# Kernel optimization log

Measured on AMD Instinct MI355X. Metric: run time of the kernel, lower is better.

The kernel has to match this reference:

```python
import jax, jax.numpy as jnp
import numpy as np

K = 16  # neighbors, from self.k in the module


def _pconv(x, w, b):
    # 1x1 Conv1d: x (B,C,N), w (O,C), b (O,)
    return jnp.einsum('oc,bcn->bon', w, x) + b[None, :, None]


def _gather_neighbors(xn, idx):
    # xn (B,N,C), idx (B,N,K) int -> (B,N,K,C)
    return jax.vmap(lambda xb, ib: xb[ib])(xn, idx)


def _local_maxpool(x, idx):
    # x (B,C,N) -> (B,N,C): max over K gathered neighbor features
    xn = jnp.transpose(x, (0, 2, 1))
    return jnp.max(_gather_neighbors(xn, idx), axis=2)


def setup_inputs() -> dict:
    key = jax.random.key(0)
    ks = jax.random.split(key, 20)
    B, N = 8, 2048
    def w(k, shape, fan_in):
        return jax.random.normal(k, shape, dtype=jnp.float32) / np.sqrt(fan_in)
    inp = {
        'pts': jax.random.normal(ks[0], (B, N, 3), dtype=jnp.float32),
        'w1a': w(ks[1], (64, 12), 12), 'b1a': jnp.zeros((64,), jnp.float32),
        'w1b': w(ks[2], (64, 64), 64), 'b1b': jnp.zeros((64,), jnp.float32),
        'w1c': w(ks[3], (64, 64), 64), 'b1c': jnp.zeros((64,), jnp.float32),
        'lin1_w': w(ks[4], (64, 64), 64), 'lin1_b': jnp.zeros((64,), jnp.float32),
        'conv1_w': w(ks[5], (128, 64), 64), 'conv1_b': jnp.zeros((128,), jnp.float32),
        'lin2_w': w(ks[6], (128, 128), 128), 'lin2_b': jnp.zeros((128,), jnp.float32),
        'conv2_w': w(ks[7], (1024, 128), 128), 'conv2_b': jnp.zeros((1024,), jnp.float32),
        'w2a': w(ks[8], (512, 1024), 1024), 'b2a': jnp.zeros((512,), jnp.float32),
        'w2b': w(ks[9], (512, 512), 512), 'b2b': jnp.zeros((512,), jnp.float32),
    }
    return inp


def reference(pts, w1a, b1a, w1b, b1b, w1c, b1c, lin1_w, lin1_b,
              conv1_w, conv1_b, lin2_w, lin2_b, conv2_w, conv2_b,
              w2a, b2a, w2b, b2b):
    B, N, _ = pts.shape
    pts_t = jnp.transpose(pts, (0, 2, 1))  # (B,3,N)
    # kNN: topk of negative squared pairwise distance (self is first neighbor)
    sq = jnp.sum(pts_t * pts_t, axis=1)                      # (B,N)
    inner = jnp.einsum('bdn,bdm->bnm', pts_t, pts_t)         # (B,N,N)
    neg_dist = 2.0 * inner - sq[:, :, None] - sq[:, None, :]
    idx = jax.lax.top_k(neg_dist, K)[1]                      # (B,N,K) int32
    # local_cov: outer product of first two gathered neighbor coords
    neigh = _gather_neighbors(pts, idx)                      # (B,N,K,3)
    cov = jnp.einsum('bni,bnj->bnij', neigh[:, :, 0], neigh[:, :, 1])
    cov = cov.reshape(B, N, 9)
    x = jnp.concatenate([pts_t, jnp.transpose(cov, (0, 2, 1))], axis=1)  # (B,12,N)
    # mlp1
    x = jax.nn.relu(_pconv(x, w1a, b1a))
    x = jax.nn.relu(_pconv(x, w1b, b1b))
    x = jax.nn.relu(_pconv(x, w1c, b1c))
    # graph layer
    x = _local_maxpool(x, idx)                               # (B,N,64)
    x = x @ lin1_w.T + lin1_b                                # (B,N,64)
    x = jnp.transpose(x, (0, 2, 1))                          # (B,64,N)
    x = jax.nn.relu(_pconv(x, conv1_w, conv1_b))             # (B,128,N)
    x = _local_maxpool(x, idx)                               # (B,N,128)
    x = x @ lin2_w.T + lin2_b
    x = jnp.transpose(x, (0, 2, 1))                          # (B,128,N)
    x = _pconv(x, conv2_w, conv2_b)                          # (B,1024,N)
    # global max pool
    x = jnp.max(x, axis=2, keepdims=True)                    # (B,1024,1)
    # mlp2
    x = jax.nn.relu(_pconv(x, w2a, b2a))
    x = _pconv(x, w2b, b2b)                                  # (B,512,1)
    return jnp.transpose(x, (0, 2, 1))                       # (B,1,512)
```

## Files before the change

kernel.cpp:

```cpp
#include <hip/hip_runtime.h>

#define BB 8
#define NN 2048
#define KK 16
#define QT 64
#define NSLICE 8
#define SLEN 256
#define KP 18

typedef short bf16x8 __attribute__((ext_vector_type(8)));
typedef float f32x4 __attribute__((ext_vector_type(4)));
typedef unsigned short ushort8v __attribute__((ext_vector_type(8)));

__device__ __forceinline__ float4 f4max(float4 a, float4 b) {
  return make_float4(fmaxf(a.x, b.x), fmaxf(a.y, b.y), fmaxf(a.z, b.z), fmaxf(a.w, b.w));
}

__device__ __forceinline__ unsigned short f2bf(float x) {
  union { float f; unsigned u; } v; v.f = x;
  unsigned r = v.u + 0x7fffu + ((v.u >> 16) & 1u);
  return (unsigned short)(r >> 16);
}
__device__ __forceinline__ float bf2f(unsigned short h) {
  union { unsigned u; float f; } v; v.u = ((unsigned)h) << 16;
  return v.f;
}

__global__ __launch_bounds__(512) void knn_kernel(
    const float* __restrict__ pts, int* __restrict__ knn_idx,
    const float* __restrict__ lin1_w, const float* __restrict__ lin1_b,
    const float* __restrict__ conv1_w, const float* __restrict__ conv1_b,
    const float* __restrict__ lin2_w, const float* __restrict__ lin2_b,
    const float* __restrict__ conv2_w, const float* __restrict__ conv2_b,
    unsigned short* __restrict__ w1hi, unsigned short* __restrict__ w1lo,
    float* __restrict__ b1p,
    unsigned short* __restrict__ w2hi, unsigned short* __restrict__ w2lo,
    float* __restrict__ b2p) {
  __shared__ float4 sp[NN];
  __shared__ unsigned char  pk[NSLICE][QT][KP];
  __shared__ float          s1v[4][QT][17];
  __shared__ unsigned short s1i[4][QT][17];
  const int tid = threadIdx.x;

  if (blockIdx.x >= 256) {
    const int gt = (blockIdx.x - 256) * 512 + tid;
    if (gt < 8192) {
      const int o = gt >> 6, c = gt & 63;
      float acc = 0.f;
#pragma unroll 8
      for (int k = 0; k < 64; ++k) acc += conv1_w[o * 64 + k] * lin1_w[k * 64 + c];
      const unsigned short h = f2bf(acc);
      w1hi[o * 64 + c] = h;
      w1lo[o * 64 + c] = f2bf(acc - bf2f(h));
      if (c == 0) {
        float bb = conv1_b[o];
        for (int k = 0; k < 64; ++k) bb += conv1_w[o * 64 + k] * lin1_b[k];
        b1p[o] = bb;
      }
    } else if (gt < 8192 + 131072) {
      const int t2 = gt - 8192;
      const int o = t2 >> 7, c = t2 & 127;
      float acc = 0.f;
#pragma unroll 8
      for (int k = 0; k < 128; ++k) acc += conv2_w[o * 128 + k] * lin2_w[k * 128 + c];
      const unsigned short h = f2bf(acc);
      w2hi[o * 128 + c] = h;
      w2lo[o * 128 + c] = f2bf(acc - bf2f(h));
      if (c == 0) {
        float bb = conv2_b[o];
        for (int k = 0; k < 128; ++k) bb += conv2_w[o * 128 + k] * lin2_b[k];
        b2p[o] = bb;
      }
    }
    return;
  }

  const int b = blockIdx.x & 7;
  const int tile = blockIdx.x >> 3;
  const int q = tid & 63;
  const int s = tid >> 6;

  for (int i = tid; i < NN; i += 512) {
    float x = pts[(size_t)(b * NN + i) * 3 + 0];
    float y = pts[(size_t)(b * NN + i) * 3 + 1];
    float z = pts[(size_t)(b * NN + i) * 3 + 2];
    sp[i] = make_float4(x, y, z, x * x + y * y + z * z);
  }
  __syncthreads();

  {
    const float4 pq = sp[tile * QT + q];
    const float qx = 2.f * pq.x, qy = 2.f * pq.y, qz = 2.f * pq.z;
    unsigned qk[KP];
#pragma unroll
    for (int j = 0; j < KP; ++j) qk[j] = 0u;
    const int m0 = s * SLEN;
    for (int mb = 0; mb < SLEN; mb += 8) {
      float4 c[8];
#pragma unroll
      for (int u = 0; u < 8; ++u) c[u] = sp[m0 + mb + u];
#pragma unroll
      for (int u = 0; u < 8; ++u) {
        const float v = fmaf(qx, c[u].x, fmaf(qy, c[u].y, fmaf(qz, c[u].z, -c[u].w)));
        unsigned uu = __float_as_uint(v);
        unsigned key = uu ^ ((unsigned)(((int)uu) >> 31) | 0x80000000u);
        unsigned run = (key & 0xFFFFFF00u) | (unsigned)(255 - (mb + u));
#pragma unroll
        for (int j = 0; j < KP; ++j) {
          const unsigned hi = max(qk[j], run);
          const unsigned lo = min(qk[j], run);
          qk[j] = hi; run = lo;
        }
      }
    }
#pragma unroll
    for (int j = 0; j < KP; ++j) pk[s][q][j] = (unsigned char)(qk[j] & 0xFFu);
  }
  __syncthreads();

  if (tid < 256) {
    const int q2 = tid & 63, pr = tid >> 6;
    const float4 pm = sp[tile * QT + q2];
    const float qx = 2.f * pm.x, qy = 2.f * pm.y, qz = 2.f * pm.z;
    float mv[16]; int mi[16];
#pragma unroll
    for (int j = 0; j < 16; ++j) { mv[j] = -3.0e38f; mi[j] = 0; }
#pragma unroll 1
    for (int ss = 2 * pr; ss <= 2 * pr + 1; ++ss) {
      const int base = ss * SLEN;
#pragma unroll 1
      for (int j = 0; j < KP; ++j) {
        const int id = base + 255 - (int)pk[ss][q2][j];
        const float4 c = sp[id];
        const float v = fmaf(qx, c.x, fmaf(qy, c.y, fmaf(qz, c.z, -c.w)));
        if (v <= mv[15]) break;
        mv[15] = v; mi[15] = id;
#pragma unroll
        for (int t = 15; t > 0; --t) {
          if (mv[t] > mv[t - 1]) {
            float tv = mv[t]; mv[t] = mv[t - 1]; mv[t - 1] = tv;
            int ti = mi[t]; mi[t] = mi[t - 1]; mi[t - 1] = ti;
          }
        }
      }
    }
#pragma unroll
    for (int j = 0; j < 16; ++j) {
      s1v[pr][q2][j] = mv[j];
      s1i[pr][q2][j] = (unsigned short)mi[j];
    }
  }
  __syncthreads();

  if (tid < QT) {
    float mv[16]; int mi[16];
#pragma unroll
    for (int j = 0; j < 16; ++j) { mv[j] = -3.0e38f; mi[j] = 0; }
#pragma unroll 1
    for (int pr = 0; pr < 4; ++pr) {
#pragma unroll 1
      for (int j = 0; j < 16; ++j) {
        const float v = s1v[pr][tid][j];
        if (v <= mv[15]) break;
        const int id = s1i[pr][tid][j];
        mv[15] = v; mi[15] = id;
#pragma unroll
        for (int t = 15; t > 0; --t) {
          if (mv[t] > mv[t - 1]) {
            float tv = mv[t]; mv[t] = mv[t - 1]; mv[t - 1] = tv;
            int ti = mi[t]; mi[t] = mi[t - 1]; mi[t - 1] = ti;
          }
        }
      }
    }
    const int nq = tile * QT + tid;
#pragma unroll
    for (int j = 0; j < 16; ++j) knn_idx[(size_t)(b * NN + nq) * KK + j] = mi[j];
  }
}

__global__ __launch_bounds__(512, 2) void mlp1_kernel(
    const float* __restrict__ pts, const int* __restrict__ knn_idx,
    const float* __restrict__ w1a, const float* __restrict__ b1a,
    const float* __restrict__ w1b, const float* __restrict__ b1b,
    const float* __restrict__ w1c, const float* __restrict__ b1c,
    float* __restrict__ f1) {
  __shared__ float h1[64][64];
  __shared__ float h2[64][64];
  const int tid = threadIdx.x;
  const int p = tid & 63;
  const int ch = tid >> 6;
  const int b = blockIdx.x & 7;
  const int nc = blockIdx.x >> 3;
  const int bn = b * NN + nc * 64 + p;

  const int n0 = knn_idx[(size_t)bn * KK + 0];
  const int n1 = knn_idx[(size_t)bn * KK + 1];
  const float* pp = &pts[(size_t)bn * 3];
  const float* p0 = &pts[((size_t)(b << 11) + n0) * 3];
  const float* p1 = &pts[((size_t)(b << 11) + n1) * 3];
  float in[12];
  in[0] = pp[0]; in[1] = pp[1]; in[2] = pp[2];
  {
    float a0 = p0[0], a1 = p0[1], a2 = p0[2];
    float c0 = p1[0], c1 = p1[1], c2 = p1[2];
    in[3] = a0 * c0; in[4]  = a0 * c1; in[5]  = a0 * c2;
    in[6] = a1 * c0; in[7]  = a1 * c1; in[8]  = a1 * c2;
    in[9] = a2 * c0; in[10] = a2 * c1; in[11] = a2 * c2;
  }

#pragma unroll
  for (int oi = 0; oi < 8; ++oi) {
    const int o = ch * 8 + oi;
    float a = b1a[o];
#pragma unroll
    for (int c = 0; c < 12; ++c) a += w1a[o * 12 + c] * in[c];
    h1[o][p] = fmaxf(a, 0.f);
  }
  __syncthreads();

  {
    float acc[8];
#pragma unroll
    for (int oi = 0; oi < 8; ++oi) acc[oi] = b1b[ch * 8 + oi];
#pragma unroll 1
    for (int cc = 0; cc < 64; cc += 32) {
      float xr[32];
#pragma unroll
      for (int c = 0; c < 32; ++c) xr[c] = h1[cc + c][p];
#pragma unroll
      for (int oi = 0; oi < 8; ++oi) {
        const int o = ch * 8 + oi;
#pragma unroll
        for (int c = 0; c < 32; ++c) acc[oi] += w1b[o * 64 + cc + c] * xr[c];
      }
    }
    __syncthreads();
#pragma unroll
    for (int oi = 0; oi < 8; ++oi) h2[ch * 8 + oi][p] = fmaxf(acc[oi], 0.f);
  }
  __syncthreads();

  {
    float acc[8];
#pragma unroll
    for (int oi = 0; oi < 8; ++oi) acc[oi] = b1c[ch * 8 + oi];
#pragma unroll 1
    for (int cc = 0; cc < 64; cc += 32) {
      float xr[32];
#pragma unroll
      for (int c = 0; c < 32; ++c) xr[c] = h2[cc + c][p];
#pragma unroll
      for (int oi = 0; oi < 8; ++oi) {
        const int o = ch * 8 + oi;
#pragma unroll
        for (int c = 0; c < 32; ++c) acc[oi] += w1c[o * 64 + cc + c] * xr[c];
      }
    }
#pragma unroll
    for (int oi = 0; oi < 8; ++oi)
      f1[(size_t)bn * 64 + ch * 8 + oi] = fmaxf(acc[oi], 0.f);
  }
}

__global__ __launch_bounds__(256, 2) void gconv1_kernel(
    const float* __restrict__ f1, const int* __restrict__ knn_idx,
    const unsigned short* __restrict__ w1hi, const unsigned short* __restrict__ w1lo,
    const float* __restrict__ b1p, float* __restrict__ f2) {
  __shared__ __align__(16) unsigned short xls[2][64][64];
  const int b = blockIdx.x & 7, nc = blockIdx.x >> 3;
  const int tid = threadIdx.x;
  const int lane = tid & 63, wv = tid >> 6;

  {
    const int p = tid & 63, ch = tid >> 6;
    const int bn = b * NN + nc * 64 + p;
    const int4* idr = (const int4*)&knn_idx[(size_t)bn * KK];
    int4 nb4[4];
#pragma unroll
    for (int q = 0; q < 4; ++q) nb4[q] = idr[q];
    float4 mx[4];
#pragma unroll
    for (int q = 0; q < 4; ++q) mx[q] = make_float4(-3e38f, -3e38f, -3e38f, -3e38f);
#pragma unroll
    for (int j = 0; j < KK; ++j) {
      const int nb = (j & 3) == 0 ? nb4[j >> 2].x : (j & 3) == 1 ? nb4[j >> 2].y
                   : (j & 3) == 2 ? nb4[j >> 2].z : nb4[j >> 2].w;
      const float4* v = (const float4*)&f1[((size_t)(b << 11) + nb) * 64 + ch * 16];
#pragma unroll
      for (int q = 0; q < 4; ++q) mx[q] = f4max(mx[q], v[q]);
    }
    char* basep = (char*)&xls[0][0][0];
#pragma unroll
    for (int s = 0; s < 2; ++s) {
      float xv[8] = {mx[2 * s].x, mx[2 * s].y, mx[2 * s].z, mx[2 * s].w,
                     mx[2 * s + 1].x, mx[2 * s + 1].y, mx[2 * s + 1].z, mx[2 * s + 1].w};
      ushort8v hw, lw;
#pragma unroll
      for (int j = 0; j < 8; ++j) {
        unsigned short h = f2bf(xv[j]);
        hw[j] = h;
        lw[j] = f2bf(xv[j] - bf2f(h));
      }
      const int slot = ch * 2 + s;
      const int swz = slot ^ (p & 7);
      char* dst = basep + p * 128 + swz * 16;
      *(ushort8v*)dst = hw;
      *(ushort8v*)(dst + 8192) = lw;
    }
  }
  __syncthreads();

  const int g = lane >> 4, r = lane & 15;
  const char* basep = (const char*)&xls[0][0][0];
  bf16x8 ah[4][2], al[4][2];
#pragma unroll
  for (int m = 0; m < 4; ++m) {
    const int row = m * 16 + r;
#pragma unroll
    for (int kt = 0; kt < 2; ++kt) {
      const int swz = (kt * 4 + g) ^ (row & 7);
      const char* p = basep + row * 128 + swz * 16;
      ah[m][kt] = *(const bf16x8*)p;
      al[m][kt] = *(const bf16x8*)(p + 8192);
    }
  }
  f32x4 acc[4][2];
#pragma unroll
  for (int m = 0; m < 4; ++m)
#pragma unroll
    for (int nt = 0; nt < 2; ++nt) acc[m][nt] = (f32x4){0.f, 0.f, 0.f, 0.f};

#pragma unroll
  for (int nt = 0; nt < 2; ++nt) {
    const int o = (wv * 2 + nt) * 16 + r;
    const char* wb = (const char*)w1hi + (size_t)o * 128 + g * 16;
    const char* lb = (const char*)w1lo + (size_t)o * 128 + g * 16;
    bf16x8 bh[2], bl[2];
#pragma unroll
    for (int kt = 0; kt < 2; ++kt) {
      bh[kt] = *(const bf16x8*)(wb + kt * 64);
      bl[kt] = *(const bf16x8*)(lb + kt * 64);
    }
#pragma unroll
    for (int kt = 0; kt < 2; ++kt) {
#pragma unroll
      for (int m = 0; m < 4; ++m) {
        acc[m][nt] = __builtin_amdgcn_mfma_f32_16x16x32_bf16(ah[m][kt], bh[kt], acc[m][nt], 0, 0, 0);
        acc[m][nt] = __builtin_amdgcn_mfma_f32_16x16x32_bf16(ah[m][kt], bl[kt], acc[m][nt], 0, 0, 0);
        acc[m][nt] = __builtin_amdgcn_mfma_f32_16x16x32_bf16(al[m][kt], bh[kt], acc[m][nt], 0, 0, 0);
      }
    }
  }
#pragma unroll
  for (int nt = 0; nt < 2; ++nt) {
    const int o = (wv * 2 + nt) * 16 + r;
    const float bias = b1p[o];
#pragma unroll
    for (int m = 0; m < 4; ++m) {
#pragma unroll
      for (int j = 0; j < 4; ++j) {
        const int row = m * 16 + g * 4 + j;
        f2[((size_t)(b * NN + nc * 64 + row)) * 128 + o] = fmaxf(acc[m][nt][j] + bias, 0.f);
      }
    }
  }
}

__global__ __launch_bounds__(256, 2) void gconv2max_kernel(
    const float* __restrict__ f2, const int* __restrict__ knn_idx,
    const unsigned short* __restrict__ w2hi, const unsigned short* __restrict__ w2lo,
    float* __restrict__ pmax) {
  __shared__ __align__(16) unsigned short xls[2][64][128];
  const int b = blockIdx.x & 7, nc = blockIdx.x >> 3;
  const int tid = threadIdx.x;
  const int lane = tid & 63, wv = tid >> 6;

  {
    const int p = tid & 63, ch = tid >> 6;
    const int bn = b * NN + nc * 64 + p;
    const int4* idr = (const int4*)&knn_idx[(size_t)bn * KK];
    int4 nb4[4];
#pragma unroll
    for (int q = 0; q < 4; ++q) nb4[q] = idr[q];
    float4 mx[8];
#pragma unroll
    for (int q = 0; q < 8; ++q) mx[q] = make_float4(-3e38f, -3e38f, -3e38f, -3e38f);
#pragma unroll
    for (int j = 0; j < KK; ++j) {
      const int nb = (j & 3) == 0 ? nb4[j >> 2].x : (j & 3) == 1 ? nb4[j >> 2].y
                   : (j & 3) == 2 ? nb4[j >> 2].z : nb4[j >> 2].w;
      const float4* v = (const float4*)&f2[((size_t)(b << 11) + nb) * 128 + ch * 32];
#pragma unroll
      for (int q = 0; q < 8; ++q) mx[q] = f4max(mx[q], v[q]);
    }
    char* basep = (char*)&xls[0][0][0];
#pragma unroll
    for (int s = 0; s < 4; ++s) {
      float xv[8] = {mx[2 * s].x, mx[2 * s].y, mx[2 * s].z, mx[2 * s].w,
                     mx[2 * s + 1].x, mx[2 * s + 1].y, mx[2 * s + 1].z, mx[2 * s + 1].w};
      ushort8v hw, lw;
#pragma unroll
      for (int j = 0; j < 8; ++j) {
        unsigned short h = f2bf(xv[j]);
        hw[j] = h;
        lw[j] = f2bf(xv[j] - bf2f(h));
      }
      const int slot = ch * 4 + s;
      const int swz = slot ^ (p & 15);
      char* dst = basep + p * 256 + swz * 16;
      *(ushort8v*)dst = hw;
      *(ushort8v*)(dst + 16384) = lw;
    }
  }
  __syncthreads();

  const int g = lane >> 4, r = lane & 15;
  const char* basep = (const char*)&xls[0][0][0];
  float omax[16];
#pragma unroll
  for (int ot = 0; ot < 16; ++ot) omax[ot] = -3e38f;

#pragma unroll
  for (int mg = 0; mg < 2; ++mg) {
    bf16x8 ah[2][4], al[2][4];
#pragma unroll
    for (int m = 0; m < 2; ++m) {
      const int row = (mg * 2 + m) * 16 + r;
#pragma unroll
      for (int kt = 0; kt < 4; ++kt) {
        const int swz = (kt * 4 + g) ^ (row & 15);
        const char* p = basep + row * 256 + swz * 16;
        ah[m][kt] = *(const bf16x8*)p;
        al[m][kt] = *(const bf16x8*)(p + 16384);
      }
    }
#pragma unroll 1
    for (int ot = 0; ot < 16; ++ot) {
      const int o = wv * 256 + ot * 16 + r;
      const char* wb = (const char*)w2hi + (size_t)o * 256 + g * 16;
      const char* lb = (const char*)w2lo + (size_t)o * 256 + g * 16;
      bf16x8 bh[4], bl[4];
#pragma unroll
      for (int kt = 0; kt < 4; ++kt) {
        bh[kt] = *(const bf16x8*)(wb + kt * 64);
        bl[kt] = *(const bf16x8*)(lb + kt * 64);
      }
      f32x4 acc0 = {0.f, 0.f, 0.f, 0.f}, acc1 = {0.f, 0.f, 0.f, 0.f};
#pragma unroll
      for (int kt = 0; kt < 4; ++kt) {
        acc0 = __builtin_amdgcn_mfma_f32_16x16x32_bf16(ah[0][kt], bh[kt], acc0, 0, 0, 0);
        acc1 = __builtin_amdgcn_mfma_f32_16x16x32_bf16(ah[1][kt], bh[kt], acc1, 0, 0, 0);
        acc0 = __builtin_amdgcn_mfma_f32_16x16x32_bf16(ah[0][kt], bl[kt], acc0, 0, 0, 0);
        acc1 = __builtin_amdgcn_mfma_f32_16x16x32_bf16(ah[1][kt], bl[kt], acc1, 0, 0, 0);
        acc0 = __builtin_amdgcn_mfma_f32_16x16x32_bf16(al[0][kt], bh[kt], acc0, 0, 0, 0);
        acc1 = __builtin_amdgcn_mfma_f32_16x16x32_bf16(al[1][kt], bh[kt], acc1, 0, 0, 0);
      }
      float mx = fmaxf(fmaxf(fmaxf(acc0[0], acc0[1]), fmaxf(acc0[2], acc0[3])),
                       fmaxf(fmaxf(acc1[0], acc1[1]), fmaxf(acc1[2], acc1[3])));
      omax[ot] = fmaxf(omax[ot], mx);
    }
  }
#pragma unroll
  for (int ot = 0; ot < 16; ++ot) {
    float v = omax[ot];
    v = fmaxf(v, __shfl_xor(v, 16, 64));
    v = fmaxf(v, __shfl_xor(v, 32, 64));
    omax[ot] = v;
  }
  if (lane < 16) {
#pragma unroll
    for (int ot = 0; ot < 16; ++ot) {
      const int o = wv * 256 + ot * 16 + lane;
      pmax[((size_t)b * 1024 + o) * 32 + nc] = omax[ot];
    }
  }
}

__global__ __launch_bounds__(256) void head_g_kernel(
    const float* __restrict__ pmax, const float* __restrict__ b2p,
    float* __restrict__ gbuf) {
  const int b = blockIdx.x & 7;
  const int o = (blockIdx.x >> 3) * 256 + threadIdx.x;
  const float4* p = (const float4*)&pmax[((size_t)b * 1024 + o) * 32];
  float4 a4 = p[0];
#pragma unroll
  for (int gi = 1; gi < 8; ++gi) a4 = f4max(a4, p[gi]);
  gbuf[b * 1024 + o] = fmaxf(fmaxf(a4.x, a4.y), fmaxf(a4.z, a4.w)) + b2p[o];
}

__global__ __launch_bounds__(256) void head_a_kernel(
    const float* __restrict__ gbuf, const float* __restrict__ w2a,
    const float* __restrict__ b2a, float* __restrict__ hbuf) {
  const int b = blockIdx.x & 7;
  const int k = (blockIdx.x >> 3) * 4 + (threadIdx.x >> 6);
  const int lane = threadIdx.x & 63;
  const float4* wr = (const float4*)&w2a[(size_t)k * 1024];
  const float4* gv = (const float4*)&gbuf[b * 1024];
  float a = 0.f;
#pragma unroll
  for (int i = 0; i < 4; ++i) {
    float4 w = wr[lane + i * 64], xx = gv[lane + i * 64];
    a += w.x * xx.x + w.y * xx.y + w.z * xx.z + w.w * xx.w;
  }
#pragma unroll
  for (int s = 32; s >= 1; s >>= 1) a += __shfl_xor(a, s, 64);
  if (lane == 0) hbuf[b * 512 + k] = fmaxf(a + b2a[k], 0.f);
}

__global__ __launch_bounds__(256) void head_b_kernel(
    const float* __restrict__ hbuf, const float* __restrict__ w2b,
    const float* __restrict__ b2b, float* __restrict__ out) {
  const int b = blockIdx.x & 7;
  const int k = (blockIdx.x >> 3) * 4 + (threadIdx.x >> 6);
  const int lane = threadIdx.x & 63;
  const float4* wr = (const float4*)&w2b[(size_t)k * 512];
  const float4* hv = (const float4*)&hbuf[b * 512];
  float a = 0.f;
#pragma unroll
  for (int i = 0; i < 2; ++i) {
    float4 w = wr[lane + i * 64], xx = hv[lane + i * 64];
    a += w.x * xx.x + w.y * xx.y + w.z * xx.z + w.w * xx.w;
  }
#pragma unroll
  for (int s = 32; s >= 1; s >>= 1) a += __shfl_xor(a, s, 64);
  if (lane == 0) out[b * 512 + k] = a + b2b[k];
}

extern "C" void kernel_launch(void* const* d_in, const int* in_sizes, int n_in,
                              void* d_out, int out_size, void* d_ws, size_t ws_size,
                              hipStream_t stream) {
  const float* pts     = (const float*)d_in[0];
  const float* w1a     = (const float*)d_in[1];
  const float* b1a     = (const float*)d_in[2];
  const float* w1b     = (const float*)d_in[3];
  const float* b1b     = (const float*)d_in[4];
  const float* w1c     = (const float*)d_in[5];
  const float* b1c     = (const float*)d_in[6];
  const float* lin1_w  = (const float*)d_in[7];
  const float* lin1_b  = (const float*)d_in[8];
  const float* conv1_w = (const float*)d_in[9];
  const float* conv1_b = (const float*)d_in[10];
  const float* lin2_w  = (const float*)d_in[11];
  const float* lin2_b  = (const float*)d_in[12];
  const float* conv2_w = (const float*)d_in[13];
  const float* conv2_b = (const float*)d_in[14];
  const float* w2a     = (const float*)d_in[15];
  const float* b2a     = (const float*)d_in[16];
  const float* w2b     = (const float*)d_in[17];
  const float* b2b     = (const float*)d_in[18];

  char* ws = (char*)d_ws;
  int*   knn_idx = (int*)ws;
  float* f1  = (float*)(ws + (1u << 20));
  float* pm  = (float*)(ws + (5u << 20));
  unsigned short* w2hi = (unsigned short*)(ws + (6u << 20));
  unsigned short* w2lo = (unsigned short*)(ws + (6u << 20) + (1u << 18));
  unsigned short* w1hi = (unsigned short*)(ws + (6u << 20) + (2u << 18));
  unsigned short* w1lo = (unsigned short*)(ws + (6u << 20) + (2u << 18) + (1u << 14));
  float* b1p = (float*)(ws + (6u << 20) + (2u << 18) + (2u << 14));
  float* b2p = (float*)(ws + (6u << 20) + (2u << 18) + (3u << 14));
  float* gbuf = (float*)(ws + (7u << 20));
  float* hbuf = (float*)(ws + (7u << 20) + (1u << 16));
  float* f2  = (float*)(ws + (9u << 20));

  knn_kernel   <<<544, 512, 0, stream>>>(pts, knn_idx,
                                         lin1_w, lin1_b, conv1_w, conv1_b,
                                         lin2_w, lin2_b, conv2_w, conv2_b,
                                         w1hi, w1lo, b1p, w2hi, w2lo, b2p);
  mlp1_kernel  <<<256, 512, 0, stream>>>(pts, knn_idx, w1a, b1a, w1b, b1b, w1c, b1c, f1);
  gconv1_kernel<<<256, 256, 0, stream>>>(f1, knn_idx, w1hi, w1lo, b1p, f2);
  gconv2max_kernel<<<256, 256, 0, stream>>>(f2, knn_idx, w2hi, w2lo, pm);
  head_g_kernel<<<32, 256, 0, stream>>>(pm, b2p, gbuf);
  head_a_kernel<<<1024, 256, 0, stream>>>(gbuf, w2a, b2a, hbuf);
  head_b_kernel<<<1024, 256, 0, stream>>>(hbuf, w2b, b2b, (float*)d_out);
}
```

Baseline: 169.6 us.

## Split kNN candidate scan across two halves of points with separate merge kernel

Splits the kNN candidate scan so each block handles only half the point set (1024 candidates), doubling the number of scanning blocks from 256 to 512. Each half writes its partial top-16 values and indices to global memory, and a new merge kernel combines the two lists into the final knn_idx. This is meant to raise occupancy and parallelism on a large GPU where 256 blocks underfill the device. In exchange it adds an extra kernel launch and a global round trip for the partial results. The per-slice index packing still uses 255-(mb+u) with 128-long slices, which stays correct but wastes key bits.

```diff
diff --git a/kernel.cpp b/kernel.cpp
--- a/kernel.cpp
+++ b/kernel.cpp
@@ -4,8 +4,8 @@
 #define NN 2048
 #define KK 16
 #define QT 64
-#define NSLICE 8
-#define SLEN 256
+#define HSLICE 8
+#define HSLEN 128
 #define KP 18
 
 typedef short bf16x8 __attribute__((ext_vector_type(8)));
@@ -26,8 +26,9 @@
   return v.f;
 }
 
-__global__ __launch_bounds__(512) void knn_kernel(
-    const float* __restrict__ pts, int* __restrict__ knn_idx,
+__global__ __launch_bounds__(512) void knn_scan_kernel(
+    const float* __restrict__ pts,
+    float* __restrict__ halfv, unsigned short* __restrict__ halfi,
     const float* __restrict__ lin1_w, const float* __restrict__ lin1_b,
     const float* __restrict__ conv1_w, const float* __restrict__ conv1_b,
     const float* __restrict__ lin2_w, const float* __restrict__ lin2_b,
@@ -36,14 +37,15 @@
     float* __restrict__ b1p,
     unsigned short* __restrict__ w2hi, unsigned short* __restrict__ w2lo,
     float* __restrict__ b2p) {
-  __shared__ float4 sp[NN];
-  __shared__ unsigned char  pk[NSLICE][QT][KP];
+  __shared__ float4 sp[1024];
+  __shared__ float4 qp[QT];
+  __shared__ unsigned char  pk[HSLICE][QT][KP];
   __shared__ float          s1v[4][QT][17];
   __shared__ unsigned short s1i[4][QT][17];
   const int tid = threadIdx.x;
 
-  if (blockIdx.x >= 256) {
-    const int gt = (blockIdx.x - 256) * 512 + tid;
+  if (blockIdx.x >= 512) {
+    const int gt = (blockIdx.x - 512) * 512 + tid;
     if (gt < 8192) {
       const int o = gt >> 6, c = gt & 63;
       float acc = 0.f;
@@ -76,32 +78,36 @@
   }
 
   const int b = blockIdx.x & 7;
-  const int tile = blockIdx.x >> 3;
+  const int t2 = blockIdx.x >> 3;
+  const int tile = t2 >> 1;
+  const int half = t2 & 1;
   const int q = tid & 63;
   const int s = tid >> 6;
 
-  for (int i = tid; i < NN; i += 512) {
-    float x = pts[(size_t)(b * NN + i) * 3 + 0];
-    float y = pts[(size_t)(b * NN + i) * 3 + 1];
-    float z = pts[(size_t)(b * NN + i) * 3 + 2];
-    sp[i] = make_float4(x, y, z, x * x + y * y + z * z);
+  for (int i = tid; i < 1024; i += 512) {
+    const size_t gi = (size_t)(b * NN + half * 1024 + i) * 3;
+    float x = pts[gi + 0], y = pts[gi + 1], z = pts[gi + 2];
+    sp[i] = make_float4(x, y, z, fmaf(x, x, fmaf(y, y, z * z)));
+  }
+  if (tid < QT) {
+    const size_t gq = (size_t)(b * NN + tile * QT + tid) * 3;
+    qp[tid] = make_float4(2.f * pts[gq + 0], 2.f * pts[gq + 1], 2.f * pts[gq + 2], 0.f);
   }
   __syncthreads();
 
   {
-    const float4 pq = sp[tile * QT + q];
-    const float qx = 2.f * pq.x, qy = 2.f * pq.y, qz = 2.f * pq.z;
+    const float4 pq = qp[q];
     unsigned qk[KP];
 #pragma unroll
     for (int j = 0; j < KP; ++j) qk[j] = 0u;
-    const int m0 = s * SLEN;
-    for (int mb = 0; mb < SLEN; mb += 8) {
+    const int m0 = s * HSLEN;
+    for (int mb = 0; mb < HSLEN; mb += 8) {
       float4 c[8];
 #pragma unroll
       for (int u = 0; u < 8; ++u) c[u] = sp[m0 + mb + u];
 #pragma unroll
       for (int u = 0; u < 8; ++u) {
-        const float v = fmaf(qx, c[u].x, fmaf(qy, c[u].y, fmaf(qz, c[u].z, -c[u].w)));
+        const float v = fmaf(pq.x, c[u].x, fmaf(pq.y, c[u].y, fmaf(pq.z, c[u].z, -c[u].w)));
         unsigned uu = __float_as_uint(v);
         unsigned key = uu ^ ((unsigned)(((int)uu) >> 31) | 0x80000000u);
         unsigned run = (key & 0xFFFFFF00u) | (unsigned)(255 - (mb + u));
@@ -120,19 +126,18 @@
 
   if (tid < 256) {
     const int q2 = tid & 63, pr = tid >> 6;
-    const float4 pm = sp[tile * QT + q2];
-    const float qx = 2.f * pm.x, qy = 2.f * pm.y, qz = 2.f * pm.z;
+    const float4 pq = qp[q2];
     float mv[16]; int mi[16];
 #pragma unroll
     for (int j = 0; j < 16; ++j) { mv[j] = -3.0e38f; mi[j] = 0; }
 #pragma unroll 1
     for (int ss = 2 * pr; ss <= 2 * pr + 1; ++ss) {
-      const int base = ss * SLEN;
+      const int base = ss * HSLEN;
 #pragma unroll 1
       for (int j = 0; j < KP; ++j) {
         const int id = base + 255 - (int)pk[ss][q2][j];
         const float4 c = sp[id];
-        const float v = fmaf(qx, c.x, fmaf(qy, c.y, fmaf(qz, c.z, -c.w)));
+        const float v = fmaf(pq.x, c.x, fmaf(pq.y, c.y, fmaf(pq.z, c.z, -c.w)));
         if (v <= mv[15]) break;
         mv[15] = v; mi[15] = id;
 #pragma unroll
@@ -173,10 +178,43 @@
         }
       }
     }
-    const int nq = tile * QT + tid;
-#pragma unroll
-    for (int j = 0; j < 16; ++j) knn_idx[(size_t)(b * NN + nq) * KK + j] = mi[j];
-  }
+    const size_t bn = (size_t)(b * NN + tile * QT + tid);
+#pragma unroll
+    for (int j = 0; j < 16; ++j) {
+      halfv[bn * 32 + half * 16 + j] = mv[j];
+      halfi[bn * 32 + half * 16 + j] = (unsigned short)(half * 1024 + mi[j]);
+    }
+  }
+}
+
+__global__ __launch_bounds__(128) void knn_merge_kernel(
+    const float* __restrict__ halfv, const unsigned short* __restrict__ halfi,
+    int* __restrict__ knn_idx) {
+  const size_t bn = (size_t)blockIdx.x * 128 + threadIdx.x;
+  const float* hv = &halfv[bn * 32];
+  const unsigned short* hi = &halfi[bn * 32];
+  float mv[16]; int mi[16];
+#pragma unroll
+  for (int j = 0; j < 16; ++j) { mv[j] = -3.0e38f; mi[j] = 0; }
+#pragma unroll 1
+  for (int h = 0; h < 2; ++h) {
+#pragma unroll 1
+    for (int j = 0; j < 16; ++j) {
+      const float v = hv[h * 16 + j];
+      if (v <= mv[15]) break;
+      const int id = hi[h * 16 + j];
+      mv[15] = v; mi[15] = id;
+#pragma unroll
+      for (int t = 15; t > 0; --t) {
+        if (mv[t] > mv[t - 1]) {
+          float tv = mv[t]; mv[t] = mv[t - 1]; mv[t - 1] = tv;
+          int ti = mi[t]; mi[t] = mi[t - 1]; mi[t - 1] = ti;
+        }
+      }
+    }
+  }
+#pragma unroll
+  for (int j = 0; j < 16; ++j) knn_idx[bn * KK + j] = mi[j];
 }
 
 __global__ __launch_bounds__(512, 2) void mlp1_kernel(
@@ -563,11 +601,14 @@
   float* gbuf = (float*)(ws + (7u << 20));
   float* hbuf = (float*)(ws + (7u << 20) + (1u << 16));
   float* f2  = (float*)(ws + (9u << 20));
-
-  knn_kernel   <<<544, 512, 0, stream>>>(pts, knn_idx,
-                                         lin1_w, lin1_b, conv1_w, conv1_b,
-                                         lin2_w, lin2_b, conv2_w, conv2_b,
-                                         w1hi, w1lo, b1p, w2hi, w2lo, b2p);
+  float* halfv = (float*)(ws + (17u << 20));
+  unsigned short* halfi = (unsigned short*)(ws + (19u << 20));
+
+  knn_scan_kernel<<<784, 512, 0, stream>>>(pts, halfv, halfi,
+                                           lin1_w, lin1_b, conv1_w, conv1_b,
+                                           lin2_w, lin2_b, conv2_w, conv2_b,
+                                           w1hi, w1lo, b1p, w2hi, w2lo, b2p);
+  knn_merge_kernel<<<128, 128, 0, stream>>>(halfv, halfi, knn_idx);
   mlp1_kernel  <<<256, 512, 0, stream>>>(pts, knn_idx, w1a, b1a, w1b, b1b, w1c, b1c, f1);
   gconv1_kernel<<<256, 256, 0, stream>>>(f1, knn_idx, w1hi, w1lo, b1p, f2);
   gconv2max_kernel<<<256, 256, 0, stream>>>(f2, knn_idx, w2hi, w2lo, pm);
```

Result: slower. 191.1 us (+12.7%).
